# Kernel optimization log

Hardware: AMD Instinct MI355X
Metric: run time of the kernel (lower is better)

The kernel has to match this reference:

```python
import jax, jax.numpy as jnp
import numpy as np
from jax import lax

DIM = 128
TOPW = 4
SCALE = DIM ** (-0.5)


def setup_inputs() -> dict:
    key = jax.random.key(0)
    kq, ki = jax.random.split(key)
    query = jax.random.normal(kq, (4, 4096, DIM), dtype=jnp.float32)
    image = jax.random.normal(ki, (4, 8192, DIM), dtype=jnp.float32)
    return {"query": query, "image": image}


def reference(query, image):
    # diff_routing=False: inputs are detached in torch; no effect on fwd values.
    # attn: (b, Nq, mn) = scaled QK^T
    attn = jnp.einsum('bqc,bmc->bqm', query, image) * SCALE
    _, topw_index = lax.top_k(attn, TOPW)  # (b, Nq, topw)
    return topw_index
```

## Files before the change

### kernel.cpp

```cpp
#include <hip/hip_runtime.h>
#include <float.h>
#include <stdint.h>


#define NBATCH 4
#define NQ 4096
#define NM 8192
#define KD 128

typedef unsigned short ushort_t;
typedef __attribute__((ext_vector_type(8))) short bf16x8;
typedef __attribute__((ext_vector_type(4))) float f32x4;

#define BETTER64(v, i, w, j) (((v) > (w)) || ((v) == (w) && (i) < (j)))

__device__ inline float fmed3(float a, float b, float c) {
#if __has_builtin(__builtin_amdgcn_fmed3f)
  return __builtin_amdgcn_fmed3f(a, b, c);
#else
  return fmaxf(fminf(a, b), fminf(fmaxf(a, b), c));
#endif
}

__device__ inline ushort_t f2bf(float f) {
  unsigned u = __float_as_uint(f);
  u += 0x7fffu + ((u >> 16) & 1u);
  return (ushort_t)(u >> 16);
}

__global__ __launch_bounds__(256) void wr_cvt(const float* __restrict__ qry,
                                              const float* __restrict__ img,
                                              ushort_t* __restrict__ qb,
                                              int4* __restrict__ ib) {
  const int blk = (int)blockIdx.x;
  const int tid = (int)threadIdx.x;
  if (blk < 2048) {
    const int t = blk * 256 + tid;
    const float4 v = ((const float4*)qry)[t];
    ushort4 o;
    o.x = f2bf(v.x); o.y = f2bf(v.y); o.z = f2bf(v.z); o.w = f2bf(v.w);
    ((ushort4*)qb)[t] = o;
  } else {
    const int tg = blk - 2048;
    const int b = tg >> 8;
    const int tile = tg & 255;
    __shared__ __align__(16) ushort_t T[32 * 128];
    {
      const int r = tid >> 3;
      const int seg = tid & 7;
      const float* src = img + ((size_t)(b * NM + tile * 32 + r)) * KD + seg * 16;
      ushort_t tmp[16];
#pragma unroll
      for (int i = 0; i < 4; ++i) {
        const float4 v = ((const float4*)src)[i];
        tmp[i * 4 + 0] = f2bf(v.x);
        tmp[i * 4 + 1] = f2bf(v.y);
        tmp[i * 4 + 2] = f2bf(v.z);
        tmp[i * 4 + 3] = f2bf(v.w);
      }
      const int c0 = (seg * 16 + r * 8) & 127;
      const int c1 = (seg * 16 + 8 + r * 8) & 127;
      *(int4*)&T[r * 128 + c0] = *(const int4*)&tmp[0];
      *(int4*)&T[r * 128 + c1] = *(const int4*)&tmp[8];
    }
    __syncthreads();
    int4* dstt = ib + ((size_t)b * 256 + tile) * 512;
#pragma unroll
    for (int h = 0; h < 2; ++h) {
      const int n = tid + h * 256;
      const int l = n & 63;
      const int ks = (n >> 6) & 3;
      const int htl = n >> 8;
      const int row = htl * 16 + (l & 15);
      const int col = ks * 32 + (l >> 4) * 8;
      dstt[n] = *(const int4*)&T[row * 128 + ((col + row * 8) & 127)];
    }
  }
}

__global__ __launch_bounds__(512, 1) void wr_mfma(const float* __restrict__ qry,
                                                  const float* __restrict__ img,
                                                  const ushort_t* __restrict__ qb,
                                                  const int4* __restrict__ ib,
                                                  int* __restrict__ out) {
  const int bid = (int)blockIdx.x;
  const int b = (bid & 7) >> 1;
  const int qt = ((bid >> 3) << 1) | (bid & 1);
  const int qbase = qt * 64;

  const int tid = (int)threadIdx.x;
  const int lane = tid & 63;
  const int w = tid >> 6;
  const int q15 = lane & 15;
  const int quad = lane >> 4;

  const ushort_t* Qb = qb + ((size_t)b * NQ + qbase) * KD;
  const int4* ibc = ib + (size_t)b * 131072;

  bf16x8 bfrag[4][4];
#pragma unroll
  for (int s = 0; s < 4; ++s)
#pragma unroll
    for (int ks = 0; ks < 4; ++ks)
      bfrag[s][ks] =
          *(const bf16x8*)(Qb + (size_t)(s * 16 + q15) * KD + ks * 32 + quad * 8);

  float tch[4][4];
#pragma unroll
  for (int s = 0; s < 4; ++s)
#pragma unroll
    for (int e = 0; e < 4; ++e) tch[s][e] = -FLT_MAX;

  bf16x8 B0[4], B1[4], B2[4];

  auto loadH = [&](bf16x8* R, int h) {
    const int4* p = ibc + (((w * 64 + h) << 8) + lane);
#pragma unroll
    for (int ks = 0; ks < 4; ++ks) R[ks] = *(const bf16x8*)(p + ks * 64);
  };

  int hl = 3;
  int vb = 2047 - 4 * quad;

  auto step = [&](bf16x8* R) {
    f32x4 a[4];
#pragma unroll
    for (int s = 0; s < 4; ++s) a[s] = {0.f, 0.f, 0.f, 0.f};
#pragma unroll
    for (int ks = 0; ks < 4; ++ks)
#pragma unroll
      for (int s = 0; s < 4; ++s)
        a[s] = __builtin_amdgcn_mfma_f32_16x16x32_bf16(R[ks], bfrag[s][ks], a[s],
                                                       0, 0, 0);
    if (hl < 64) loadH(R, hl);
    ++hl;
#pragma unroll
    for (int s = 0; s < 4; ++s) {
#pragma unroll
      for (int r = 0; r < 4; ++r) {
        const unsigned kr = (unsigned)(vb - r);
        const float k =
            __uint_as_float((__float_as_uint(a[s][r]) & 0xFFFFF800u) | kr);
        tch[s][3] = fmed3(k, tch[s][2], tch[s][3]);
        tch[s][2] = fmed3(k, tch[s][1], tch[s][2]);
        tch[s][1] = fmed3(k, tch[s][0], tch[s][1]);
        tch[s][0] = fmaxf(tch[s][0], k);
      }
    }
    vb -= 16;
  };

  loadH(B0, 0);
  loadH(B1, 1);
  loadH(B2, 2);
  for (int g = 0; g < 21; ++g) { step(B0); step(B1); step(B2); }
  step(B0);

#pragma unroll
  for (int s = 0; s < 4; ++s) {
    float k4[4];
#pragma unroll
    for (int e = 0; e < 4; ++e) k4[e] = __shfl_down(tch[s][e], 32, 64);
#pragma unroll
    for (int e = 0; e < 4; ++e) {
      const float k = k4[e];
      tch[s][3] = fmed3(k, tch[s][2], tch[s][3]);
      tch[s][2] = fmed3(k, tch[s][1], tch[s][2]);
      tch[s][1] = fmed3(k, tch[s][0], tch[s][1]);
      tch[s][0] = fmaxf(tch[s][0], k);
    }
#pragma unroll
    for (int e = 0; e < 4; ++e) k4[e] = __shfl_down(tch[s][e], 16, 64);
#pragma unroll
    for (int e = 0; e < 4; ++e) {
      const float k = k4[e];
      tch[s][3] = fmed3(k, tch[s][2], tch[s][3]);
      tch[s][2] = fmed3(k, tch[s][1], tch[s][2]);
      tch[s][1] = fmed3(k, tch[s][0], tch[s][1]);
      tch[s][0] = fmaxf(tch[s][0], k);
    }
  }

  __shared__ float ck[64][33];
  __shared__ int top8[64][8];
  __shared__ double pd[64][8];
  __shared__ int pi[64][8];

  if (lane < 16) {
#pragma unroll
    for (int s = 0; s < 4; ++s)
#pragma unroll
      for (int e = 0; e < 4; ++e) ck[s * 16 + q15][w * 4 + e] = tch[s][e];
  }
  __syncthreads();

  for (int p = tid; p < 2048; p += 512) {
    const int q = p >> 5;
    const int j = p & 31;
    const float k = ck[q][j];
    int rank = 0;
#pragma unroll 8
    for (int i = 0; i < 32; ++i) {
      const float o = ck[q][i];
      rank += (o > k) || (o == k && i < j);
    }
    if (rank < 8) {
      const unsigned bits = __float_as_uint(k);
      top8[q][rank] = (j >> 2) * 1024 + 2047 - (int)(bits & 0x7FFu);
    }
  }
  __syncthreads();

  {
    const int q = tid >> 3;
    const int slot = tid & 7;
    const int m = top8[q][slot];
    const float* qrow = qry + ((size_t)b * NQ + qbase + q) * KD;
    const float* irow = img + ((size_t)b * NM + m) * KD;
    double s0 = 0.0, s1 = 0.0, s2 = 0.0, s3 = 0.0;
#pragma unroll
    for (int k = 0; k < KD; k += 4) {
      const float4 xv = *(const float4*)(qrow + k);
      const float4 yv = *(const float4*)(irow + k);
      s0 = fma((double)xv.x, (double)yv.x, s0);
      s1 = fma((double)xv.y, (double)yv.y, s1);
      s2 = fma((double)xv.z, (double)yv.z, s2);
      s3 = fma((double)xv.w, (double)yv.w, s3);
    }
    pd[q][slot] = (s0 + s1) + (s2 + s3);
    pi[q][slot] = m;
  }
  __syncthreads();

  if (tid < 64) {
    const int q = tid;
    double fv[4];
    int fi[4];
#pragma unroll
    for (int e = 0; e < 4; ++e) { fv[e] = -DBL_MAX; fi[e] = 0x7fffffff; }
    for (int sl = 0; sl < 8; ++sl) {
      const double v = pd[q][sl];
      const int m = pi[q][sl];
      const bool b0 = BETTER64(v, m, fv[0], fi[0]);
      const bool b1 = BETTER64(v, m, fv[1], fi[1]);
      const bool b2 = BETTER64(v, m, fv[2], fi[2]);
      const bool b3 = BETTER64(v, m, fv[3], fi[3]);
      fv[3] = b2 ? fv[2] : (b3 ? v : fv[3]);
      fi[3] = b2 ? fi[2] : (b3 ? m : fi[3]);
      fv[2] = b1 ? fv[1] : (b2 ? v : fv[2]);
      fi[2] = b1 ? fi[1] : (b2 ? m : fi[2]);
      fv[1] = b0 ? fv[0] : (b1 ? v : fv[1]);
      fi[1] = b0 ? fi[0] : (b1 ? m : fi[1]);
      fv[0] = b0 ? v : fv[0];
      fi[0] = b0 ? m : fi[0];
    }
    int4 o;
    o.x = fi[0]; o.y = fi[1]; o.z = fi[2]; o.w = fi[3];
    *(int4*)(out + ((size_t)b * NQ + qbase + q) * 4) = o;
  }
}

#define QT 64
#define MT 128
#define KC 64
#define NTHREADS 512

__global__ __launch_bounds__(NTHREADS) void wr_main(const float* __restrict__ qry,
                                                    const float* __restrict__ img,
                                                    int* __restrict__ out) {
  __shared__ __align__(16) float A_lds[KD * QT];
  __shared__ __align__(16) float B_lds[KC * MT];

  const int t = (int)threadIdx.x;
  const int b = (int)blockIdx.x >> 6;
  const int qbase = ((int)blockIdx.x & 63) * QT;

  const float* qp = qry + ((size_t)b * NQ + qbase) * KD;
  const float* ip = img + (size_t)b * NM * KD;

  {
    const int r = t >> 3;
    const int kc = t & 7;
    const float* src = qp + (size_t)r * KD;
#pragma unroll
    for (int i = 0; i < 4; ++i) {
      const int k0 = kc * 4 + i * 32;
      const float4 v = *(const float4*)(src + k0);
      A_lds[(k0 + 0) * QT + r] = v.x;
      A_lds[(k0 + 1) * QT + r] = v.y;
      A_lds[(k0 + 2) * QT + r] = v.z;
      A_lds[(k0 + 3) * QT + r] = v.w;
    }
  }

  const int qi = t >> 5;
  const int mi = t & 31;

  float tv[4][4];
  int ti[4][4];
#pragma unroll
  for (int j = 0; j < 4; ++j)
#pragma unroll
    for (int s = 0; s < 4; ++s) { tv[j][s] = -FLT_MAX; ti[j][s] = 0x7fffffff; }

  for (int tile = 0; tile < NM / MT; ++tile) {
    const int mbase = tile * MT;
    float acc[4][4];
#pragma unroll
    for (int j = 0; j < 4; ++j)
#pragma unroll
      for (int s = 0; s < 4; ++s) acc[j][s] = 0.0f;

    for (int kb = 0; kb < KD; kb += KC) {
      __syncthreads();
      {
        const int r = t >> 2;
        const int kc = t & 3;
        const float* src = ip + (size_t)(mbase + r) * KD + kb;
#pragma unroll
        for (int i = 0; i < 4; ++i) {
          const int k0 = kc * 4 + i * 16;
          const float4 v = *(const float4*)(src + k0);
          B_lds[(k0 + 0) * MT + r] = v.x;
          B_lds[(k0 + 1) * MT + r] = v.y;
          B_lds[(k0 + 2) * MT + r] = v.z;
          B_lds[(k0 + 3) * MT + r] = v.w;
        }
      }
      __syncthreads();

#pragma unroll 8
      for (int k = 0; k < KC; ++k) {
        const float4 av = *(const float4*)&A_lds[(kb + k) * QT + qi * 4];
        const float4 bv = *(const float4*)&B_lds[k * MT + mi * 4];
        acc[0][0] = fmaf(av.x, bv.x, acc[0][0]);
        acc[0][1] = fmaf(av.x, bv.y, acc[0][1]);
        acc[0][2] = fmaf(av.x, bv.z, acc[0][2]);
        acc[0][3] = fmaf(av.x, bv.w, acc[0][3]);
        acc[1][0] = fmaf(av.y, bv.x, acc[1][0]);
        acc[1][1] = fmaf(av.y, bv.y, acc[1][1]);
        acc[1][2] = fmaf(av.y, bv.z, acc[1][2]);
        acc[1][3] = fmaf(av.y, bv.w, acc[1][3]);
        acc[2][0] = fmaf(av.z, bv.x, acc[2][0]);
        acc[2][1] = fmaf(av.z, bv.y, acc[2][1]);
        acc[2][2] = fmaf(av.z, bv.z, acc[2][2]);
        acc[2][3] = fmaf(av.z, bv.w, acc[2][3]);
        acc[3][0] = fmaf(av.w, bv.x, acc[3][0]);
        acc[3][1] = fmaf(av.w, bv.y, acc[3][1]);
        acc[3][2] = fmaf(av.w, bv.z, acc[3][2]);
        acc[3][3] = fmaf(av.w, bv.w, acc[3][3]);
      }
    }

#pragma unroll
    for (int j = 0; j < 4; ++j) {
#pragma unroll
      for (int s = 0; s < 4; ++s) {
        const float v = acc[j][s];
        const int m = mbase + mi * 4 + s;
        const bool b0 = v > tv[j][0];
        const bool b1 = v > tv[j][1];
        const bool b2 = v > tv[j][2];
        const bool b3 = v > tv[j][3];
        tv[j][3] = b2 ? tv[j][2] : (b3 ? v : tv[j][3]);
        ti[j][3] = b2 ? ti[j][2] : (b3 ? m : ti[j][3]);
        tv[j][2] = b1 ? tv[j][1] : (b2 ? v : tv[j][2]);
        ti[j][2] = b1 ? ti[j][1] : (b2 ? m : ti[j][2]);
        tv[j][1] = b0 ? tv[j][0] : (b1 ? v : tv[j][1]);
        ti[j][1] = b0 ? ti[j][0] : (b1 ? m : ti[j][1]);
        tv[j][0] = b0 ? v : tv[j][0];
        ti[j][0] = b0 ? m : ti[j][0];
      }
    }
  }

  __syncthreads();
  int* idx_lds = (int*)B_lds;
#pragma unroll
  for (int j = 0; j < 4; ++j)
#pragma unroll
    for (int s = 0; s < 4; ++s)
      idx_lds[(qi * 4 + j) * 128 + mi * 4 + s] = ti[j][s];
  __syncthreads();

  double* pv = (double*)A_lds;
  int* piL = (int*)(A_lds + 4096);
  {
    const int r = t >> 3;
    const int slot = t & 7;
    const float* qrow = qp + (size_t)r * KD;
    double bv[4];
    int bi[4];
#pragma unroll
    for (int e = 0; e < 4; ++e) { bv[e] = -DBL_MAX; bi[e] = 0x7fffffff; }

    for (int c = 0; c < 16; ++c) {
      const int m = idx_lds[r * 128 + slot * 16 + c];
      const float* irow = ip + (size_t)m * KD;
      double s0 = 0.0, s1 = 0.0, s2 = 0.0, s3 = 0.0;
#pragma unroll
      for (int k = 0; k < KD; k += 4) {
        const float4 xv = *(const float4*)(qrow + k);
        const float4 yv = *(const float4*)(irow + k);
        s0 = fma((double)xv.x, (double)yv.x, s0);
        s1 = fma((double)xv.y, (double)yv.y, s1);
        s2 = fma((double)xv.z, (double)yv.z, s2);
        s3 = fma((double)xv.w, (double)yv.w, s3);
      }
      const double v = (s0 + s1) + (s2 + s3);
      const bool b0 = BETTER64(v, m, bv[0], bi[0]);
      const bool b1 = BETTER64(v, m, bv[1], bi[1]);
      const bool b2 = BETTER64(v, m, bv[2], bi[2]);
      const bool b3 = BETTER64(v, m, bv[3], bi[3]);
      bv[3] = b2 ? bv[2] : (b3 ? v : bv[3]);
      bi[3] = b2 ? bi[2] : (b3 ? m : bi[3]);
      bv[2] = b1 ? bv[1] : (b2 ? v : bv[2]);
      bi[2] = b1 ? bi[1] : (b2 ? m : bi[2]);
      bv[1] = b0 ? bv[0] : (b1 ? v : bv[1]);
      bi[1] = b0 ? bi[0] : (b1 ? m : bi[1]);
      bv[0] = b0 ? v : bv[0];
      bi[0] = b0 ? m : bi[0];
    }
#pragma unroll
    for (int e = 0; e < 4; ++e) {
      pv[t * 4 + e] = bv[e];
      piL[t * 4 + e] = bi[e];
    }
  }
  __syncthreads();

  if (t < QT) {
    double fv[4];
    int fi[4];
#pragma unroll
    for (int e = 0; e < 4; ++e) { fv[e] = -DBL_MAX; fi[e] = 0x7fffffff; }
    for (int sl = 0; sl < 8; ++sl) {
#pragma unroll
      for (int e = 0; e < 4; ++e) {
        const double v = pv[(t * 8 + sl) * 4 + e];
        const int m = piL[(t * 8 + sl) * 4 + e];
        const bool b0 = BETTER64(v, m, fv[0], fi[0]);
        const bool b1 = BETTER64(v, m, fv[1], fi[1]);
        const bool b2 = BETTER64(v, m, fv[2], fi[2]);
        const bool b3 = BETTER64(v, m, fv[3], fi[3]);
        fv[3] = b2 ? fv[2] : (b3 ? v : fv[3]);
        fi[3] = b2 ? fi[2] : (b3 ? m : fi[3]);
        fv[2] = b1 ? fv[1] : (b2 ? v : fv[2]);
        fi[2] = b1 ? fi[1] : (b2 ? m : fi[2]);
        fv[1] = b0 ? fv[0] : (b1 ? v : fv[1]);
        fi[1] = b0 ? fi[0] : (b1 ? m : fi[1]);
        fv[0] = b0 ? v : fv[0];
        fi[0] = b0 ? m : fi[0];
      }
    }
    int4 o;
    o.x = fi[0]; o.y = fi[1]; o.z = fi[2]; o.w = fi[3];
    *(int4*)(out + ((size_t)b * NQ + qbase + t) * 4) = o;
  }
}

extern "C" void kernel_launch(void* const* d_in, const int* in_sizes, int n_in,
                              void* d_out, int out_size, void* d_ws, size_t ws_size,
                              hipStream_t stream) {
  const float* qry = (const float*)d_in[0];
  const float* img = (const float*)d_in[1];
  int* out = (int*)d_out;

  const size_t qbBytes = (size_t)NBATCH * NQ * KD * sizeof(ushort_t);
  const size_t ibBytes = (size_t)NBATCH * NM * KD * sizeof(ushort_t);

  if (ws_size >= qbBytes + ibBytes) {
    ushort_t* qb = (ushort_t*)d_ws;
    int4* ib = (int4*)((char*)d_ws + qbBytes);
    wr_cvt<<<3072, 256, 0, stream>>>(qry, img, qb, ib);
    wr_mfma<<<256, 512, 0, stream>>>(qry, img, qb, ib, out);
  } else {
    wr_main<<<NBATCH * (NQ / QT), NTHREADS, 0, stream>>>(qry, img, out);
  }
}
```

Measured before the change: 133.0 us.

## Split MFMA top-k into candidate kernel plus separate rerank merge kernel

Replaces the single 256-block MFMA kernel with a 1024-block candidate pass that splits the image dimension four ways. Each wave keeps a per-row top-4 of bf16 scores, with the index packed into the low mantissa bits, and writes 64 candidates per query row to workspace. A separate merge kernel ranks those candidates, takes the top 8, rescores them exactly in fp64 from the fp32 inputs, and writes the final top-4. This raises occupancy and parallelism at the cost of an extra launch, a candidate buffer round-trip, and a larger workspace requirement; if the workspace is too small, the old path is used.

```diff
diff --git a/kernel.cpp b/kernel.cpp
--- a/kernel.cpp
+++ b/kernel.cpp
@@ -78,11 +78,211 @@
   }
 }
 
-__global__ __launch_bounds__(512, 1) void wr_mfma(const float* __restrict__ qry,
-                                                  const float* __restrict__ img,
-                                                  const ushort_t* __restrict__ qb,
-                                                  const int4* __restrict__ ib,
-                                                  int* __restrict__ out) {
+__global__ __launch_bounds__(256, 3) void wr_mfma_c(const ushort_t* __restrict__ qb,
+                                                    const int4* __restrict__ ib,
+                                                    float* __restrict__ candKeys) {
+  const int bid = (int)blockIdx.x;
+  const int mq = bid & 3;
+  const int qt = (bid >> 2) & 63;
+  const int b = bid >> 8;
+  const int qbase = qt * 64;
+
+  const int tid = (int)threadIdx.x;
+  const int lane = tid & 63;
+  const int w = tid >> 6;
+  const int q15 = lane & 15;
+  const int quad = lane >> 4;
+
+  const ushort_t* Qb = qb + ((size_t)b * NQ + qbase) * KD;
+  const int4* ibc = ib + (size_t)b * 131072;
+  const int H0 = mq * 128 + w * 32;
+
+  bf16x8 bfrag[4][4];
+#pragma unroll
+  for (int s = 0; s < 4; ++s)
+#pragma unroll
+    for (int ks = 0; ks < 4; ++ks)
+      bfrag[s][ks] =
+          *(const bf16x8*)(Qb + (size_t)(s * 16 + q15) * KD + ks * 32 + quad * 8);
+
+  float tch[4][4];
+#pragma unroll
+  for (int s = 0; s < 4; ++s)
+#pragma unroll
+    for (int e = 0; e < 4; ++e) tch[s][e] = -FLT_MAX;
+
+  bf16x8 B0[4], B1[4], B2[4];
+
+  auto loadH = [&](bf16x8* R, int t) {
+    const int4* p = ibc + (((H0 + t) << 8) + lane);
+#pragma unroll
+    for (int ks = 0; ks < 4; ++ks) R[ks] = *(const bf16x8*)(p + ks * 64);
+  };
+
+  int hl = 3;
+  int vb = 2047 - 4 * quad;
+
+  auto step = [&](bf16x8* R) {
+    f32x4 a[4];
+#pragma unroll
+    for (int s = 0; s < 4; ++s) a[s] = {0.f, 0.f, 0.f, 0.f};
+#pragma unroll
+    for (int ks = 0; ks < 4; ++ks)
+#pragma unroll
+      for (int s = 0; s < 4; ++s)
+        a[s] = __builtin_amdgcn_mfma_f32_16x16x32_bf16(R[ks], bfrag[s][ks], a[s],
+                                                       0, 0, 0);
+    if (hl < 32) loadH(R, hl);
+    ++hl;
+#pragma unroll
+    for (int s = 0; s < 4; ++s) {
+#pragma unroll
+      for (int r = 0; r < 4; ++r) {
+        const unsigned kr = (unsigned)(vb - r);
+        const float k =
+            __uint_as_float((__float_as_uint(a[s][r]) & 0xFFFFF800u) | kr);
+        tch[s][3] = fmed3(k, tch[s][2], tch[s][3]);
+        tch[s][2] = fmed3(k, tch[s][1], tch[s][2]);
+        tch[s][1] = fmed3(k, tch[s][0], tch[s][1]);
+        tch[s][0] = fmaxf(tch[s][0], k);
+      }
+    }
+    vb -= 16;
+  };
+
+  loadH(B0, 0);
+  loadH(B1, 1);
+  loadH(B2, 2);
+  for (int g = 0; g < 10; ++g) { step(B0); step(B1); step(B2); }
+  step(B0);
+  step(B1);
+
+#pragma unroll
+  for (int s = 0; s < 4; ++s) {
+    float k4[4];
+#pragma unroll
+    for (int e = 0; e < 4; ++e) k4[e] = __shfl_down(tch[s][e], 32, 64);
+#pragma unroll
+    for (int e = 0; e < 4; ++e) {
+      const float k = k4[e];
+      tch[s][3] = fmed3(k, tch[s][2], tch[s][3]);
+      tch[s][2] = fmed3(k, tch[s][1], tch[s][2]);
+      tch[s][1] = fmed3(k, tch[s][0], tch[s][1]);
+      tch[s][0] = fmaxf(tch[s][0], k);
+    }
+#pragma unroll
+    for (int e = 0; e < 4; ++e) k4[e] = __shfl_down(tch[s][e], 16, 64);
+#pragma unroll
+    for (int e = 0; e < 4; ++e) {
+      const float k = k4[e];
+      tch[s][3] = fmed3(k, tch[s][2], tch[s][3]);
+      tch[s][2] = fmed3(k, tch[s][1], tch[s][2]);
+      tch[s][1] = fmed3(k, tch[s][0], tch[s][1]);
+      tch[s][0] = fmaxf(tch[s][0], k);
+    }
+  }
+
+  if (lane < 16) {
+    const int w16 = mq * 4 + w;
+#pragma unroll
+    for (int s = 0; s < 4; ++s) {
+      const int rowG = (b * 64 + qt) * 64 + s * 16 + q15;
+      float4 v;
+      v.x = tch[s][0]; v.y = tch[s][1]; v.z = tch[s][2]; v.w = tch[s][3];
+      *(float4*)&candKeys[(size_t)rowG * 64 + w16 * 4] = v;
+    }
+  }
+}
+
+__global__ __launch_bounds__(256) void wr_merge(const float* __restrict__ qry,
+                                                const float* __restrict__ img,
+                                                const float* __restrict__ candKeys,
+                                                int* __restrict__ out) {
+  const int tid = (int)threadIdx.x;
+  const int rowBase = (int)blockIdx.x * 32;
+
+  __shared__ float ckL[32][64];
+  __shared__ int top8L[32][8];
+  __shared__ double pdL[32][8];
+  __shared__ int piL[32][8];
+
+  for (int idx = tid; idx < 2048; idx += 256)
+    ckL[idx >> 6][idx & 63] = candKeys[(size_t)rowBase * 64 + idx];
+  __syncthreads();
+
+  const int r = tid >> 3;
+  const int slot = tid & 7;
+
+#pragma unroll
+  for (int h = 0; h < 8; ++h) {
+    const int j = slot * 8 + h;
+    const float k = ckL[r][j];
+    int rank = 0;
+#pragma unroll 16
+    for (int i = 0; i < 64; ++i) {
+      const float o = ckL[r][i];
+      rank += (o > k) || (o == k && i < j);
+    }
+    if (rank < 8) {
+      const unsigned bits = __float_as_uint(k);
+      top8L[r][rank] = (j >> 2) * 512 + 2047 - (int)(bits & 0x7FFu);
+    }
+  }
+  __syncthreads();
+
+  {
+    const int rowG = rowBase + r;
+    const int m = top8L[r][slot];
+    const float* qrow = qry + (size_t)rowG * KD;
+    const float* irow = img + ((size_t)(rowG >> 12) * NM + m) * KD;
+    double s0 = 0.0, s1 = 0.0, s2 = 0.0, s3 = 0.0;
+#pragma unroll
+    for (int k = 0; k < KD; k += 4) {
+      const float4 xv = *(const float4*)(qrow + k);
+      const float4 yv = *(const float4*)(irow + k);
+      s0 = fma((double)xv.x, (double)yv.x, s0);
+      s1 = fma((double)xv.y, (double)yv.y, s1);
+      s2 = fma((double)xv.z, (double)yv.z, s2);
+      s3 = fma((double)xv.w, (double)yv.w, s3);
+    }
+    pdL[r][slot] = (s0 + s1) + (s2 + s3);
+    piL[r][slot] = m;
+  }
+  __syncthreads();
+
+  if (tid < 32) {
+    const int q = tid;
+    double fv[4];
+    int fi[4];
+#pragma unroll
+    for (int e = 0; e < 4; ++e) { fv[e] = -DBL_MAX; fi[e] = 0x7fffffff; }
+    for (int sl = 0; sl < 8; ++sl) {
+      const double v = pdL[q][sl];
+      const int m = piL[q][sl];
+      const bool b0 = BETTER64(v, m, fv[0], fi[0]);
+      const bool b1 = BETTER64(v, m, fv[1], fi[1]);
+      const bool b2 = BETTER64(v, m, fv[2], fi[2]);
+      const bool b3 = BETTER64(v, m, fv[3], fi[3]);
+      fv[3] = b2 ? fv[2] : (b3 ? v : fv[3]);
+      fi[3] = b2 ? fi[2] : (b3 ? m : fi[3]);
+      fv[2] = b1 ? fv[1] : (b2 ? v : fv[2]);
+      fi[2] = b1 ? fi[1] : (b2 ? m : fi[2]);
+      fv[1] = b0 ? fv[0] : (b1 ? v : fv[1]);
+      fi[1] = b0 ? fi[0] : (b1 ? m : fi[1]);
+      fv[0] = b0 ? v : fv[0];
+      fi[0] = b0 ? m : fi[0];
+    }
+    int4 o;
+    o.x = fi[0]; o.y = fi[1]; o.z = fi[2]; o.w = fi[3];
+    *(int4*)(out + (size_t)(rowBase + q) * 4) = o;
+  }
+}
+
+__global__ __launch_bounds__(512, 1) void wr_mfma8(const float* __restrict__ qry,
+                                                   const float* __restrict__ img,
+                                                   const ushort_t* __restrict__ qb,
+                                                   const int4* __restrict__ ib,
+                                                   int* __restrict__ out) {
   const int bid = (int)blockIdx.x;
   const int b = (bid & 7) >> 1;
   const int qt = ((bid >> 3) << 1) | (bid & 1);
@@ -468,12 +668,20 @@
 
   const size_t qbBytes = (size_t)NBATCH * NQ * KD * sizeof(ushort_t);
   const size_t ibBytes = (size_t)NBATCH * NM * KD * sizeof(ushort_t);
-
-  if (ws_size >= qbBytes + ibBytes) {
+  const size_t candBytes = (size_t)NBATCH * NQ * 64 * sizeof(float);
+
+  if (ws_size >= qbBytes + ibBytes + candBytes) {
+    ushort_t* qb = (ushort_t*)d_ws;
+    int4* ib = (int4*)((char*)d_ws + qbBytes);
+    float* candKeys = (float*)((char*)d_ws + qbBytes + ibBytes);
+    wr_cvt<<<3072, 256, 0, stream>>>(qry, img, qb, ib);
+    wr_mfma_c<<<1024, 256, 0, stream>>>(qb, ib, candKeys);
+    wr_merge<<<512, 256, 0, stream>>>(qry, img, candKeys, out);
+  } else if (ws_size >= qbBytes + ibBytes) {
     ushort_t* qb = (ushort_t*)d_ws;
     int4* ib = (int4*)((char*)d_ws + qbBytes);
     wr_cvt<<<3072, 256, 0, stream>>>(qry, img, qb, ib);
-    wr_mfma<<<256, 512, 0, stream>>>(qry, img, qb, ib, out);
+    wr_mfma8<<<256, 512, 0, stream>>>(qry, img, qb, ib, out);
   } else {
     wr_main<<<NBATCH * (NQ / QT), NTHREADS, 0, stream>>>(qry, img, out);
   }
```

New measurement: 182.9 us. 1.37x slower.
